# Performance work log

Measured on AMD Instinct MI355X. Metric: run time of the kernel, lower is better.

## Reference

```python
import jax, jax.numpy as jnp
import numpy as np

B, S, E, H = 4, 2048, 1024, 16
D = E // H  # head dim = 64


def setup_inputs() -> dict:
    key = jax.random.key(0)
    ks = jax.random.split(key, 5)
    s = 0.02
    return {
        "x": jax.random.normal(ks[0], (B, S, E), dtype=jnp.float32),
        "Wq": jax.random.normal(ks[1], (E, E), dtype=jnp.float32) * s,
        "Wk": jax.random.normal(ks[2], (E, E), dtype=jnp.float32) * s,
        "Wv": jax.random.normal(ks[3], (E, E), dtype=jnp.float32) * s,
        "Wo": jax.random.normal(ks[4], (E, E), dtype=jnp.float32) * s,
        "bo": jnp.zeros((E,), dtype=jnp.float32),
    }


def reference(x, Wq, Wk, Wv, Wo, bo):
    b, s, e = x.shape
    h, d = H, e // H
    # QKV projections -> [b, h, s, d]
    q = (x @ Wq).reshape(b, s, h, d).transpose(0, 2, 1, 3)
    k = (x @ Wk).reshape(b, s, h, d).transpose(0, 2, 1, 3)
    v = (x @ Wv).reshape(b, s, h, d).transpose(0, 2, 1, 3)
    # scores [b, h, s, s], causal mask with -inf, scaled softmax
    a = jnp.einsum('bhqd,bhkd->bhqk', q, k)
    causal = jnp.tril(jnp.ones((s, s), dtype=bool))  # True where allowed
    a = jnp.where(causal, a, -jnp.inf) / jnp.sqrt(jnp.asarray(d, x.dtype))
    a = jax.nn.softmax(a, axis=-1)
    # dropout p=0.0 (identity in eval)
    y = jnp.einsum('bhqk,bhkd->bhqd', a, v)
    y = y.transpose(0, 2, 1, 3).reshape(b, s, e)
    return y @ Wo + bo
```

## Files before the change

### kernel.cpp

```cpp
#include <hip/hip_runtime.h>

typedef __bf16 bf16x8 __attribute__((ext_vector_type(8)));
typedef float f32x4 __attribute__((ext_vector_type(4)));
typedef unsigned short u16x8 __attribute__((ext_vector_type(8)));

#define S_LEN 2048
#define NHEAD 16
#define HDIM  64
#define EMB   1024

__device__ __forceinline__ ushort f2b(float v) {
  union { float f; unsigned u; } x; x.f = v;
  unsigned r = (x.u + 0x7fffu + ((x.u >> 16) & 1u)) >> 16;
  return (ushort)r;
}

__device__ __forceinline__ ushort f2b_trunc(float v) {
  union { float f; unsigned u; } x; x.f = v;
  return (ushort)(x.u >> 16);
}

typedef const __attribute__((address_space(1))) unsigned int* gp1_t;
typedef __attribute__((address_space(3))) unsigned int* lp3_t;
__device__ __forceinline__ void gld16(const ushort* g, const ushort* l) {
  __builtin_amdgcn_global_load_lds((gp1_t)(unsigned long long)(uintptr_t)g,
                                   (lp3_t)(unsigned int)(uintptr_t)l, 16, 0, 0);
}

__global__ __launch_bounds__(256) void prep_kernel(
    const float* __restrict__ x, const float* __restrict__ W0,
    const float* __restrict__ W1, const float* __restrict__ W2,
    const float* __restrict__ W3, ushort* __restrict__ xb,
    ushort* __restrict__ Wt0, ushort* __restrict__ Wt1,
    ushort* __restrict__ Wt2, ushort* __restrict__ Wt3, float scale0) {
  const int z = blockIdx.z;
  if (z == 4) {
    size_t base = ((size_t)(blockIdx.y * 32 + blockIdx.x)) * 8192 + threadIdx.x * 4;
#pragma unroll
    for (int i = 0; i < 8; ++i) {
      float4 v = *(const float4*)(x + base + i * 1024);
      ushort4 o;
      o.x = f2b(v.x); o.y = f2b(v.y); o.z = f2b(v.z); o.w = f2b(v.w);
      *(ushort4*)(xb + base + i * 1024) = o;
    }
    return;
  }
  __shared__ float t[32][33];
  const float* W = z == 0 ? W0 : (z == 1 ? W1 : (z == 2 ? W2 : W3));
  ushort* Wt = z == 0 ? Wt0 : (z == 1 ? Wt1 : (z == 2 ? Wt2 : Wt3));
  const float scale = z == 0 ? scale0 : 1.0f;
  int k0 = blockIdx.x * 32, n0 = blockIdx.y * 32;
  int c = threadIdx.x & 31, r0 = threadIdx.x >> 5;
#pragma unroll
  for (int i = 0; i < 4; ++i) {
    int r = r0 + i * 8;
    t[r][c] = W[(size_t)(k0 + r) * EMB + n0 + c];
  }
  __syncthreads();
#pragma unroll
  for (int i = 0; i < 4; ++i) {
    int r = r0 + i * 8;
    Wt[(size_t)(n0 + r) * EMB + k0 + c] = f2b(t[c][r] * scale);
  }
}

template <int EPI>
__global__ __launch_bounds__(256) void gemm_kernel(
    const ushort* __restrict__ A, const ushort* __restrict__ Bt, int K, int N,
    ushort* __restrict__ outQ, ushort* __restrict__ outK, ushort* __restrict__ outVt,
    float* __restrict__ outF, const float* __restrict__ bias) {
  __shared__ ushort As[2][128 * 32];
  __shared__ ushort Bs[2][128 * 32];
  const int tid = threadIdx.x;
  const int lane = tid & 63, ln = lane & 15, quad = lane >> 4;
  const int wave = tid >> 6, wm = wave >> 1, wn = wave & 1;
  const long m0 = (long)blockIdx.x * 128, n0 = (long)blockIdx.y * 128;

  const int sr = lane >> 2, sc = (lane & 3) * 8;
  const ushort* AgL = A + (m0 + 32 * wave + sr) * (long)K + sc;
  const ushort* BgL = Bt + (n0 + 32 * wave + sr) * (long)K + sc;

  f32x4 acc[4][4] = {};
  const int KT = K >> 5;

  {
    ushort* as = &As[0][32 * wave * 32];
    ushort* bs = &Bs[0][32 * wave * 32];
    gld16(AgL, as);
    gld16(AgL + 16 * (long)K, as + 16 * 32);
    gld16(BgL, bs);
    gld16(BgL + 16 * (long)K, bs + 16 * 32);
  }
  __syncthreads();

  for (int kt = 0; kt < KT; ++kt) {
    if (kt + 1 < KT) {
      const int nb = (kt + 1) & 1;
      const ushort* a = AgL + (kt + 1) * 32;
      const ushort* b = BgL + (kt + 1) * 32;
      ushort* as = &As[nb][32 * wave * 32];
      ushort* bs = &Bs[nb][32 * wave * 32];
      gld16(a, as);
      gld16(a + 16 * (long)K, as + 16 * 32);
      gld16(b, bs);
      gld16(b + 16 * (long)K, bs + 16 * 32);
    }
    const ushort* Ac = &As[kt & 1][0];
    const ushort* Bc = &Bs[kt & 1][0];
    bf16x8 af[4], bf[4];
#pragma unroll
    for (int mt = 0; mt < 4; ++mt)
      af[mt] = *(const bf16x8*)(Ac + (wm * 64 + mt * 16 + ln) * 32 + quad * 8);
#pragma unroll
    for (int nt = 0; nt < 4; ++nt)
      bf[nt] = *(const bf16x8*)(Bc + (wn * 64 + nt * 16 + ln) * 32 + quad * 8);
#pragma unroll
    for (int mt = 0; mt < 4; ++mt)
#pragma unroll
      for (int nt = 0; nt < 4; ++nt)
        acc[mt][nt] = __builtin_amdgcn_mfma_f32_16x16x32_bf16(af[mt], bf[nt], acc[mt][nt], 0, 0, 0);
    __syncthreads();
  }

  if (EPI == 0) {
    const int sel = (int)(n0 >> 10);
    if (sel == 2) {
#pragma unroll
      for (int mt = 0; mt < 4; ++mt) {
        const long mbase = m0 + wm * 64 + mt * 16 + quad * 4;
        const long bb = mbase >> 11, s = mbase & 2047;
#pragma unroll
        for (int nt = 0; nt < 4; ++nt) {
          const int nn = (int)((n0 & 1023) + wn * 64 + nt * 16 + ln);
          const int h = nn >> 6, d = nn & 63;
          uint2 val;
          val.x = (unsigned)f2b(acc[mt][nt][0]) | ((unsigned)f2b(acc[mt][nt][1]) << 16);
          val.y = (unsigned)f2b(acc[mt][nt][2]) | ((unsigned)f2b(acc[mt][nt][3]) << 16);
          *(uint2*)(outVt + (((bb * NHEAD + h) * (long)HDIM + d) * S_LEN) + s) = val;
        }
      }
    } else {
      ushort* dst = sel == 0 ? outQ : outK;
#pragma unroll
      for (int mt = 0; mt < 4; ++mt) {
#pragma unroll
        for (int nt = 0; nt < 4; ++nt) {
          const int nn = (int)((n0 & 1023) + wn * 64 + nt * 16 + ln);
          const int h = nn >> 6, d = nn & 63;
#pragma unroll
          for (int r = 0; r < 4; ++r) {
            const long m = m0 + wm * 64 + mt * 16 + quad * 4 + r;
            const long bb = m >> 11, s = m & 2047;
            dst[(((bb * NHEAD + h) * S_LEN) + s) * HDIM + d] = f2b(acc[mt][nt][r]);
          }
        }
      }
    }
  } else {
#pragma unroll
    for (int mt = 0; mt < 4; ++mt) {
#pragma unroll
      for (int nt = 0; nt < 4; ++nt) {
#pragma unroll
        for (int r = 0; r < 4; ++r) {
          const long m = m0 + wm * 64 + mt * 16 + quad * 4 + r;
          const long n = n0 + wn * 64 + nt * 16 + ln;
          outF[m * (long)N + n] = acc[mt][nt][r] + bias[n];
        }
      }
    }
  }
}

__global__ __launch_bounds__(256) void attn_kernel(const ushort* __restrict__ Q,
                                                   const ushort* __restrict__ Kg,
                                                   const ushort* __restrict__ Vt,
                                                   ushort* __restrict__ Y) {
  __shared__ alignas(16) ushort Ks[2][2 * 64 * 32];
  __shared__ alignas(16) ushort Vs[2][2 * 64 * 32];
  __shared__ alignas(16) ushort Ps[4 * 2 * 16 * 72];
  const int tid = threadIdx.x;
  const int wave = tid >> 6, lane = tid & 63, ln = lane & 15, quad = lane >> 4;
  const int bh = blockIdx.x;
  const int qb = 15 - (int)blockIdx.y;
  const int q0 = qb * 128;
  const size_t base = (size_t)bh * S_LEN * HDIM;
  const int ntiles = 2 * qb + 2;

  const u16x8 ob = {0x3F80, 0x3F80, 0x3F80, 0x3F80, 0x3F80, 0x3F80, 0x3F80, 0x3F80};
  const bf16x8 ones = __builtin_bit_cast(bf16x8, ob);

  bf16x8 qf[2][2];
#pragma unroll
  for (int mt = 0; mt < 2; ++mt)
#pragma unroll
    for (int ks2 = 0; ks2 < 2; ++ks2)
      qf[mt][ks2] = *(const bf16x8*)(Q + base + (size_t)(q0 + wave * 32 + mt * 16 + ln) * HDIM +
                                     ks2 * 32 + quad * 8);

  f32x4 acc[2][4] = {};
  f32x4 accl[2] = {};

  const int sr = lane >> 2, sc = (lane & 3) * 8;
  const ushort* KgL = Kg + base + (size_t)(16 * wave + sr) * HDIM + sc;
  const ushort* VgL = Vt + base + (size_t)(16 * wave + sr) * S_LEN + sc;

  {
    ushort* kb = &Ks[0][16 * wave * 32];
    ushort* vb = &Vs[0][16 * wave * 32];
    gld16(KgL, kb);
    gld16(KgL + 32, kb + 2048);
    gld16(VgL, vb);
    gld16(VgL + 32, vb + 2048);
  }
  __syncthreads();

  ushort* Pw0 = Ps + wave * 2304;
  ushort* Pw1 = Pw0 + 1152;
  const int swW = (quad >> 1) << 4;
  const int swR = (ln >> 3) << 4;

  for (int kt = 0; kt < ntiles; ++kt) {
    const int cur = kt & 1;
    const int k0 = kt * 64;
    if (kt + 1 < ntiles) {
      const int nb = cur ^ 1;
      const size_t k1 = (size_t)(k0 + 64);
      ushort* kb = &Ks[nb][16 * wave * 32];
      ushort* vb = &Vs[nb][16 * wave * 32];
      gld16(KgL + k1 * HDIM, kb);
      gld16(KgL + k1 * HDIM + 32, kb + 2048);
      gld16(VgL + k1, vb);
      gld16(VgL + k1 + 32, vb + 2048);
    }
    const ushort* Kc = &Ks[cur][0];
    const ushort* Vc = &Vs[cur][0];
    const int qbase = q0 + wave * 32;

    if (k0 < qbase + 32) {
      f32x4 s0[4] = {}, s1[4] = {};
#pragma unroll
      for (int ks2 = 0; ks2 < 2; ++ks2) {
#pragma unroll
        for (int nt = 0; nt < 4; ++nt) {
          bf16x8 bk = *(const bf16x8*)(Kc + ks2 * 2048 + (nt * 16 + ln) * 32 + quad * 8);
          s0[nt] = __builtin_amdgcn_mfma_f32_16x16x32_bf16(qf[0][ks2], bk, s0[nt], 0, 0, 0);
          s1[nt] = __builtin_amdgcn_mfma_f32_16x16x32_bf16(qf[1][ks2], bk, s1[nt], 0, 0, 0);
        }
      }

      if (k0 + 63 > qbase) {
        const int rowq = qbase + quad * 4;
#pragma unroll
        for (int nt = 0; nt < 4; ++nt)
#pragma unroll
          for (int r = 0; r < 4; ++r) {
            const int key = k0 + nt * 16 + ln;
            if (key > rowq + r) s0[nt][r] = -3.0e38f;
            if (key > rowq + 16 + r) s1[nt][r] = -3.0e38f;
          }
      }

      asm volatile("" ::: "memory");
#pragma unroll
      for (int nt = 0; nt < 4; ++nt) {
#pragma unroll
        for (int r = 0; r < 4; ++r) {
          float p0 = __builtin_amdgcn_exp2f(s0[nt][r]);
          float p1 = __builtin_amdgcn_exp2f(s1[nt][r]);
          const int row = (quad * 4 + r) * 72;
          const int col = (nt * 16 + ln) ^ swW;
          Pw0[row + col] = f2b_trunc(p0);
          Pw1[row + col] = f2b_trunc(p1);
        }
      }
      asm volatile("" ::: "memory");

#pragma unroll
      for (int ks2 = 0; ks2 < 2; ++ks2) {
        const int rcol = (ks2 * 32 + quad * 8) ^ swR;
        bf16x8 ap0 = *(const bf16x8*)(Pw0 + ln * 72 + rcol);
        bf16x8 ap1 = *(const bf16x8*)(Pw1 + ln * 72 + rcol);
        accl[0] = __builtin_amdgcn_mfma_f32_16x16x32_bf16(ap0, ones, accl[0], 0, 0, 0);
        accl[1] = __builtin_amdgcn_mfma_f32_16x16x32_bf16(ap1, ones, accl[1], 0, 0, 0);
#pragma unroll
        for (int t2 = 0; t2 < 4; ++t2) {
          bf16x8 bv = *(const bf16x8*)(Vc + ks2 * 2048 + (t2 * 16 + ln) * 32 + quad * 8);
          acc[0][t2] = __builtin_amdgcn_mfma_f32_16x16x32_bf16(ap0, bv, acc[0][t2], 0, 0, 0);
          acc[1][t2] = __builtin_amdgcn_mfma_f32_16x16x32_bf16(ap1, bv, acc[1][t2], 0, 0, 0);
        }
      }
    }
    __syncthreads();
  }

  const long b = bh >> 4;
  const int h = bh & 15;
#pragma unroll
  for (int mt = 0; mt < 2; ++mt) {
#pragma unroll
    for (int r = 0; r < 4; ++r) {
      float inv = 1.0f / accl[mt][r];
      const int qq = q0 + wave * 32 + mt * 16 + quad * 4 + r;
#pragma unroll
      for (int t2 = 0; t2 < 4; ++t2)
        Y[(((b * S_LEN + qq) * NHEAD) + h) * HDIM + t2 * 16 + ln] = f2b(acc[mt][t2][r] * inv);
    }
  }
}

extern "C" void kernel_launch(void* const* d_in, const int* in_sizes, int n_in,
                              void* d_out, int out_size, void* d_ws, size_t ws_size,
                              hipStream_t stream) {
  const float* x  = (const float*)d_in[0];
  const float* Wq = (const float*)d_in[1];
  const float* Wk = (const float*)d_in[2];
  const float* Wv = (const float*)d_in[3];
  const float* Wo = (const float*)d_in[4];
  const float* bo = (const float*)d_in[5];
  float* out = (float*)d_out;

  const size_t XE = (size_t)8192 * EMB;
  ushort* ws    = (ushort*)d_ws;
  ushort* xb    = ws;
  ushort* Wtqkv = xb + XE;
  ushort* Wto   = Wtqkv + 3 * 1048576;
  ushort* Qb    = Wto + 1048576;
  ushort* Kb    = Qb + XE;
  ushort* Vtb   = Kb + XE;
  ushort* Yb    = xb;

  const float SCALE_Q = 1.4426950408889634f / 8.0f;

  prep_kernel<<<dim3(32, 32, 5), 256, 0, stream>>>(
      x, Wq, Wk, Wv, Wo, xb, Wtqkv, Wtqkv + 1048576, Wtqkv + 2097152, Wto, SCALE_Q);

  gemm_kernel<0><<<dim3(64, 24), 256, 0, stream>>>(xb, Wtqkv, EMB, 3072,
                                                   Qb, Kb, Vtb, nullptr, nullptr);
  attn_kernel<<<dim3(64, 16), 256, 0, stream>>>(Qb, Kb, Vtb, Yb);
  gemm_kernel<1><<<dim3(64, 8), 256, 0, stream>>>(Yb, Wto, EMB, EMB,
                                                  nullptr, nullptr, nullptr, out, bo);
}
```

Measured before the change: 236.2 us.

## Replace GEMM with 8-wave 128x256 tile kernel using deeper LDS pipeline

Replaces the 4-wave 128x128 GEMM with an 8-wave kernel using 128x256 output tiles and a K step of 64 split into two 32-wide halves. LDS holds multiple stages, and loads are issued ahead under explicit vmcnt waits, raw s_barrier calls and setprio around the MFMA bursts. The goal is to overlap global-to-LDS traffic with matrix math and to reuse A tiles across twice as many N columns. The cost is more LDS per block (96KB) and a hand-tuned schedule that depends on exact outstanding-load counts.

```diff
diff --git a/kernel.cpp b/kernel.cpp
--- a/kernel.cpp
+++ b/kernel.cpp
@@ -25,6 +25,12 @@
 __device__ __forceinline__ void gld16(const ushort* g, const ushort* l) {
   __builtin_amdgcn_global_load_lds((gp1_t)(unsigned long long)(uintptr_t)g,
                                    (lp3_t)(unsigned int)(uintptr_t)l, 16, 0, 0);
+}
+
+__device__ __forceinline__ void barf() {
+  asm volatile("" ::: "memory");
+  __builtin_amdgcn_s_barrier();
+  asm volatile("" ::: "memory");
 }
 
 __global__ __launch_bounds__(256) void prep_kernel(
@@ -65,61 +71,100 @@
 }
 
 template <int EPI>
-__global__ __launch_bounds__(256) void gemm_kernel(
-    const ushort* __restrict__ A, const ushort* __restrict__ Bt, int K, int N,
+__global__ __launch_bounds__(512, 2) void gemm8_kernel(
+    const ushort* __restrict__ A, const ushort* __restrict__ Bt,
     ushort* __restrict__ outQ, ushort* __restrict__ outK, ushort* __restrict__ outVt,
     float* __restrict__ outF, const float* __restrict__ bias) {
-  __shared__ ushort As[2][128 * 32];
-  __shared__ ushort Bs[2][128 * 32];
+  __shared__ ushort lds8[49152];
   const int tid = threadIdx.x;
-  const int lane = tid & 63, ln = lane & 15, quad = lane >> 4;
-  const int wave = tid >> 6, wm = wave >> 1, wn = wave & 1;
-  const long m0 = (long)blockIdx.x * 128, n0 = (long)blockIdx.y * 128;
-
-  const int sr = lane >> 2, sc = (lane & 3) * 8;
-  const ushort* AgL = A + (m0 + 32 * wave + sr) * (long)K + sc;
-  const ushort* BgL = Bt + (n0 + 32 * wave + sr) * (long)K + sc;
+  const int wave = tid >> 6, lane = tid & 63, ln = lane & 15, quad = lane >> 4;
+  const int wm = wave >> 2, wn = wave & 3;
+  const long m0 = (long)blockIdx.x * 128, n0 = (long)blockIdx.y * 256;
+  constexpr int K = EMB, KT = K / 64;
+
+  const int srow = tid >> 2;
+  const int scol = (tid & 3) * 8;
+  const ushort* srcA  = A  + (m0 + srow) * (long)K + scol;
+  const ushort* srcB0 = Bt + (n0 + srow) * (long)K + scol;
+  const ushort* srcB1 = Bt + (n0 + 128 + srow) * (long)K + scol;
+  const int dA_  = wave * 512;
+  const int dB0_ = wave * 512;
+  const int dB1_ = 4096 + wave * 512;
+
+#define STG_A(kk, par, t)                                                      \
+  gld16(srcA + (kk) * 32 + (t) * 64, lds8 + ((kk) * 2 + (par)) * 4096 + dA_)
+#define STG_B(kk, par, t)                                                      \
+  do {                                                                         \
+    gld16(srcB0 + (kk) * 32 + (t) * 64,                                        \
+          lds8 + 16384 + ((kk) * 2 + (par)) * 8192 + dB0_);                    \
+    gld16(srcB1 + (kk) * 32 + (t) * 64,                                        \
+          lds8 + 16384 + ((kk) * 2 + (par)) * 8192 + dB1_);                    \
+  } while (0)
+
+#define RD_A(kk, par)                                                          \
+  do {                                                                         \
+    const ushort* p_ = lds8 + ((kk) * 2 + (par)) * 4096 +                      \
+                       (wm * 64 + ln) * 32 + quad * 8;                         \
+    af[0] = *(const bf16x8*)p_;                                                \
+    af[1] = *(const bf16x8*)(p_ + 512);                                        \
+    af[2] = *(const bf16x8*)(p_ + 1024);                                       \
+    af[3] = *(const bf16x8*)(p_ + 1536);                                       \
+  } while (0)
+#define RD_B(kk, par)                                                          \
+  do {                                                                         \
+    const ushort* p_ = lds8 + 16384 + ((kk) * 2 + (par)) * 8192 +              \
+                       (wn * 64 + ln) * 32 + quad * 8;                         \
+    bfr[0] = *(const bf16x8*)p_;                                               \
+    bfr[1] = *(const bf16x8*)(p_ + 512);                                       \
+    bfr[2] = *(const bf16x8*)(p_ + 1024);                                      \
+    bfr[3] = *(const bf16x8*)(p_ + 1536);                                      \
+  } while (0)
+
+#define MM16()                                                                 \
+  do {                                                                         \
+    _Pragma("unroll") for (int mt = 0; mt < 4; ++mt)                           \
+        _Pragma("unroll") for (int nt = 0; nt < 4; ++nt)                       \
+            acc[mt][nt] = __builtin_amdgcn_mfma_f32_16x16x32_bf16(             \
+                af[mt], bfr[nt], acc[mt][nt], 0, 0, 0);                        \
+  } while (0)
+
+  STG_A(0, 0, 0); STG_B(0, 0, 0);
+  STG_A(1, 0, 0); STG_B(1, 0, 0);
+  STG_A(0, 1, 1); STG_B(0, 1, 1);
+  asm volatile("s_waitcnt vmcnt(3)" ::: "memory");
+  barf();
 
   f32x4 acc[4][4] = {};
-  const int KT = K >> 5;
-
-  {
-    ushort* as = &As[0][32 * wave * 32];
-    ushort* bs = &Bs[0][32 * wave * 32];
-    gld16(AgL, as);
-    gld16(AgL + 16 * (long)K, as + 16 * 32);
-    gld16(BgL, bs);
-    gld16(BgL + 16 * (long)K, bs + 16 * 32);
-  }
-  __syncthreads();
-
-  for (int kt = 0; kt < KT; ++kt) {
-    if (kt + 1 < KT) {
-      const int nb = (kt + 1) & 1;
-      const ushort* a = AgL + (kt + 1) * 32;
-      const ushort* b = BgL + (kt + 1) * 32;
-      ushort* as = &As[nb][32 * wave * 32];
-      ushort* bs = &Bs[nb][32 * wave * 32];
-      gld16(a, as);
-      gld16(a + 16 * (long)K, as + 16 * 32);
-      gld16(b, bs);
-      gld16(b + 16 * (long)K, bs + 16 * 32);
-    }
-    const ushort* Ac = &As[kt & 1][0];
-    const ushort* Bc = &Bs[kt & 1][0];
-    bf16x8 af[4], bf[4];
-#pragma unroll
-    for (int mt = 0; mt < 4; ++mt)
-      af[mt] = *(const bf16x8*)(Ac + (wm * 64 + mt * 16 + ln) * 32 + quad * 8);
-#pragma unroll
-    for (int nt = 0; nt < 4; ++nt)
-      bf[nt] = *(const bf16x8*)(Bc + (wn * 64 + nt * 16 + ln) * 32 + quad * 8);
-#pragma unroll
-    for (int mt = 0; mt < 4; ++mt)
-#pragma unroll
-      for (int nt = 0; nt < 4; ++nt)
-        acc[mt][nt] = __builtin_amdgcn_mfma_f32_16x16x32_bf16(af[mt], bf[nt], acc[mt][nt], 0, 0, 0);
-    __syncthreads();
+  bf16x8 af[4], bfr[4];
+
+#define TILE(t, par, parn)                                                     \
+  do {                                                                         \
+                                                          \
+    RD_A(0, par); RD_B(0, par);                                                \
+    if ((t) + 1 < KT) { STG_A(1, parn, (t) + 1); STG_B(1, parn, (t) + 1); }    \
+    barf();                                                                    \
+    __builtin_amdgcn_s_setprio(1);                                             \
+    MM16();                                                                    \
+    __builtin_amdgcn_s_setprio(0);                                             \
+    barf();                                                                    \
+                                                          \
+    RD_A(1, par); RD_B(1, par);                                                \
+    if ((t) + 2 < KT) { STG_A(0, par, (t) + 2); STG_B(0, par, (t) + 2); }      \
+    barf();                                                                    \
+    __builtin_amdgcn_s_setprio(1);                                             \
+    MM16();                                                                    \
+    __builtin_amdgcn_s_setprio(0);                                             \
+    if ((t) + 2 < KT) {                                                        \
+      asm volatile("s_waitcnt vmcnt(3)" ::: "memory");                         \
+    } else if ((t) + 1 < KT) {                                                 \
+      asm volatile("s_waitcnt vmcnt(0)" ::: "memory");                         \
+    }                                                                          \
+    barf();                                                                    \
+  } while (0)
+
+  for (int th = 0; th < KT; th += 2) {
+    TILE(th, 0, 1);
+    TILE(th + 1, 1, 0);
   }
 
   if (EPI == 0) {
@@ -161,15 +206,22 @@
     for (int mt = 0; mt < 4; ++mt) {
 #pragma unroll
       for (int nt = 0; nt < 4; ++nt) {
+        const long n = n0 + wn * 64 + nt * 16 + ln;
+        const float bv = bias[n];
 #pragma unroll
         for (int r = 0; r < 4; ++r) {
           const long m = m0 + wm * 64 + mt * 16 + quad * 4 + r;
-          const long n = n0 + wn * 64 + nt * 16 + ln;
-          outF[m * (long)N + n] = acc[mt][nt][r] + bias[n];
-        }
-      }
-    }
-  }
+          outF[m * (long)EMB + n] = acc[mt][nt][r] + bv;
+        }
+      }
+    }
+  }
+#undef TILE
+#undef MM16
+#undef RD_B
+#undef RD_A
+#undef STG_B
+#undef STG_A
 }
 
 __global__ __launch_bounds__(256) void attn_kernel(const ushort* __restrict__ Q,
@@ -335,9 +387,9 @@
   prep_kernel<<<dim3(32, 32, 5), 256, 0, stream>>>(
       x, Wq, Wk, Wv, Wo, xb, Wtqkv, Wtqkv + 1048576, Wtqkv + 2097152, Wto, SCALE_Q);
 
-  gemm_kernel<0><<<dim3(64, 24), 256, 0, stream>>>(xb, Wtqkv, EMB, 3072,
-                                                   Qb, Kb, Vtb, nullptr, nullptr);
+  gemm8_kernel<0><<<dim3(64, 12), 512, 0, stream>>>(xb, Wtqkv, Qb, Kb, Vtb,
+                                                    nullptr, nullptr);
   attn_kernel<<<dim3(64, 16), 256, 0, stream>>>(Qb, Kb, Vtb, Yb);
-  gemm_kernel<1><<<dim3(64, 8), 256, 0, stream>>>(Yb, Wto, EMB, EMB,
-                                                  nullptr, nullptr, nullptr, out, bo);
-}
+  gemm8_kernel<1><<<dim3(64, 4), 512, 0, stream>>>(Yb, Wto, nullptr, nullptr,
+                                                   nullptr, out, bo);
+}
```

Result: slower. 242.9 us (+2.8%).
